# Optimization experiments

Measured on AMD Instinct MI355X. Metric: run time of the kernel, lower is better.

## Reference

```python
import jax, jax.numpy as jnp
import numpy as np


def _gcn_conv(x, src, dst, num_nodes, W, b):
    """PyG GCNConv: add self-loops, symmetric normalization, scatter-add, bias."""
    h = x @ W  # [N, F_out]
    # degree over destination nodes (all edge weights are 1, incl. self-loops)
    deg = jax.ops.segment_sum(jnp.ones_like(dst, dtype=h.dtype), dst,
                              num_segments=num_nodes)
    deg_inv_sqrt = jnp.where(deg > 0, jax.lax.rsqrt(deg), 0.0)
    norm = deg_inv_sqrt[src] * deg_inv_sqrt[dst]  # [E+N]
    msg = h[src] * norm[:, None]                  # gather + scale
    out = jax.ops.segment_sum(msg, dst, num_segments=num_nodes)  # scatter-add
    return out + b


def setup_inputs() -> dict:
    key = jax.random.key(0)
    k_x, k_e, k_w1, k_w2 = jax.random.split(key, 4)
    N, E, F = 50000, 800000, 128
    x = jax.random.normal(k_x, (N, F), dtype=jnp.float32)
    edge_index = jax.random.randint(k_e, (2, E), 0, N, dtype=jnp.int64)
    scale = 1.0 / np.sqrt(F)
    W1 = jax.random.normal(k_w1, (F, F), dtype=jnp.float32) * scale
    b1 = jnp.zeros((F,), dtype=jnp.float32)
    W2 = jax.random.normal(k_w2, (F, F), dtype=jnp.float32) * scale
    b2 = jnp.zeros((F,), dtype=jnp.float32)
    return {"x": x, "edge_index": edge_index, "W1": W1, "b1": b1,
            "W2": W2, "b2": b2}


def reference(x, edge_index, W1, b1, W2, b2):
    num_nodes = x.shape[0]
    loops = jnp.arange(num_nodes, dtype=edge_index.dtype)
    src = jnp.concatenate([edge_index[0], loops])
    dst = jnp.concatenate([edge_index[1], loops])
    # layer 1: GCNConv -> Identity norm -> relu -> dropout(eval=identity)
    h = jax.nn.relu(_gcn_conv(x, src, dst, num_nodes, W1, b1))
    # layer 2 (last_activation=True, so relu again)
    out = jax.nn.relu(_gcn_conv(h, src, dst, num_nodes, W2, b2))
    return out
```

## Files before the change

kernel.cpp:

```cpp
#include <hip/hip_runtime.h>
#include <hip/hip_bf16.h>

#define CDIV(a,b) (((a)+(b)-1)/(b))

typedef __bf16 bf16x8 __attribute__((ext_vector_type(8)));
typedef float  f32x4  __attribute__((ext_vector_type(4)));

union Frag16 { uint4 u; bf16x8 f; unsigned short s[8]; };
union Pack8  { unsigned short s[4]; uint2 u; };

__device__ __forceinline__ unsigned short f2bf(float f) {
    unsigned u = __float_as_uint(f);
    return (unsigned short)((u + 0x7fff + ((u >> 16) & 1)) >> 16);
}
__device__ __forceinline__ float bf2f(unsigned short s) {
    return __uint_as_float(((unsigned)s) << 16);
}

__device__ __forceinline__ int load_src(const int* e, int f, int E, int i) {
    return f ? e[i] : e[2 * i];
}
__device__ __forceinline__ int load_dst(const int* e, int f, int E, int i) {
    return f ? e[E + i] : e[2 * (E + i)];
}

__global__ __launch_bounds__(256) void prep_kernel(const float* __restrict__ W1,
                                                   const float* __restrict__ W2,
                                                   unsigned short* __restrict__ Wf1h,
                                                   unsigned short* __restrict__ Wf1l,
                                                   unsigned short* __restrict__ Wf2h,
                                                   unsigned short* __restrict__ Wf2l,
                                                   const int* __restrict__ edges,
                                                   int* __restrict__ flag, int E,
                                                   int4* __restrict__ zero_base, int Z4) {
    int tid = threadIdx.x;
    if (blockIdx.x == 2) {
        if (tid == 0) *flag = 0;
        __syncthreads();
        int n = min(E, 4096);
        int found = 0;
        for (int j = tid; j < n; j += 256) found |= (edges[2 * j + 1] != 0);
        if (found) *flag = 1;
        return;
    }
    if (blockIdx.x >= 3) {
        int idx = (blockIdx.x - 3) * 256 + tid;
        if (idx < Z4) zero_base[idx] = make_int4(0, 0, 0, 0);
        return;
    }
    const float* W = (blockIdx.x == 0) ? W1 : W2;
    unsigned short* Wfh = (blockIdx.x == 0) ? Wf1h : Wf2h;
    unsigned short* Wfl = (blockIdx.x == 0) ? Wf1l : Wf2l;
    #pragma unroll
    for (int it = 0; it < 8; ++it) {
        int c = it * 256 + tid;
        int ntk = c >> 6;
        int lane = c & 63;
        int ks = ntk & 3;
        int ntile = ntk >> 2;
        int quad = lane >> 4, nlo = lane & 15;
        int n = ntile * 16 + nlo;
        Frag16 h, l;
        #pragma unroll
        for (int j = 0; j < 8; ++j) {
            float w = W[(ks * 32 + quad * 8 + j) * 128 + n];
            h.s[j] = f2bf(w);
            float rr = w - bf2f(h.s[j]);
            l.s[j] = f2bf(rr);
        }
        *(uint4*)(Wfh + (size_t)c * 8) = h.u;
        *(uint4*)(Wfl + (size_t)c * 8) = l.u;
    }
}

__device__ __forceinline__ void gemm_body(const float* __restrict__ X,
                                          const unsigned short* __restrict__ Wfh,
                                          const unsigned short* __restrict__ Wfl,
                                          unsigned short* __restrict__ out16,
                                          int N, int blk,
                                          unsigned short (*Xh)[136],
                                          unsigned short (*Xl)[136]) {
    int tid = threadIdx.x;
    int row0 = blk * 64;
    #pragma unroll
    for (int it = 0; it < 8; ++it) {
        int f = it * 256 + tid;
        int r = f >> 5, c4 = f & 31;
        float4 v = make_float4(0.f, 0.f, 0.f, 0.f);
        int gr = row0 + r;
        if (gr < N) v = *(const float4*)(X + (size_t)gr * 128 + c4 * 4);
        float vv[4] = {v.x, v.y, v.z, v.w};
        Pack8 h, l;
        #pragma unroll
        for (int j = 0; j < 4; ++j) {
            h.s[j] = f2bf(vv[j]);
            float rr = vv[j] - bf2f(h.s[j]);
            l.s[j] = f2bf(rr);
        }
        *(uint2*)(&Xh[r][c4 * 4]) = h.u;
        *(uint2*)(&Xl[r][c4 * 4]) = l.u;
    }
    __syncthreads();

    int lane = tid & 63;
    int wv = tid >> 6;
    int quad = lane >> 4, nlo = lane & 15;
    f32x4 acc[8];
    #pragma unroll
    for (int t = 0; t < 8; ++t) acc[t] = (f32x4){0.f, 0.f, 0.f, 0.f};

    #pragma unroll
    for (int ks = 0; ks < 4; ++ks) {
        int kcol = ks * 32 + quad * 8;
        Frag16 xh, xl;
        xh.u = *(const uint4*)(&Xh[wv * 16 + nlo][kcol]);
        xl.u = *(const uint4*)(&Xl[wv * 16 + nlo][kcol]);
        #pragma unroll
        for (int t = 0; t < 8; ++t) {
            size_t cidx = ((size_t)(t * 4 + ks) * 64 + lane) * 8;
            Frag16 wh, wl;
            wh.u = *(const uint4*)(Wfh + cidx);
            wl.u = *(const uint4*)(Wfl + cidx);
            acc[t] = __builtin_amdgcn_mfma_f32_16x16x32_bf16(xh.f, wh.f, acc[t], 0, 0, 0);
            acc[t] = __builtin_amdgcn_mfma_f32_16x16x32_bf16(xh.f, wl.f, acc[t], 0, 0, 0);
            acc[t] = __builtin_amdgcn_mfma_f32_16x16x32_bf16(xl.f, wh.f, acc[t], 0, 0, 0);
        }
    }
    #pragma unroll
    for (int rg = 0; rg < 4; ++rg) {
        int gr = row0 + wv * 16 + quad * 4 + rg;
        if (gr < N) {
            #pragma unroll
            for (int t = 0; t < 8; ++t)
                out16[(size_t)gr * 128 + t * 16 + nlo] = f2bf(acc[t][rg]);
        }
    }
}

__global__ __launch_bounds__(256) void fat_kernel(const float* __restrict__ X,
                                                  const unsigned short* __restrict__ Wfh,
                                                  const unsigned short* __restrict__ Wfl,
                                                  unsigned short* __restrict__ out16,
                                                  int N, int Ggemm,
                                                  const int* __restrict__ edges,
                                                  const int* __restrict__ flag,
                                                  int* __restrict__ counts_sh,
                                                  int* __restrict__ rank, int E) {
    __shared__ unsigned short Xh[64][136];
    __shared__ unsigned short Xl[64][136];
    if (blockIdx.x < (unsigned)Ggemm) {
        gemm_body(X, Wfh, Wfl, out16, N, blockIdx.x, Xh, Xl);
        return;
    }
    int e = (blockIdx.x - Ggemm) * 256 + threadIdx.x;
    if (e >= E) return;
    int f = *flag;
    int d = load_dst(edges, f, E, e);
    int s = blockIdx.x & 7;
    int r = atomicAdd(&counts_sh[s * N + d], 1);
    rank[e] = (r << 3) | s;
}

__global__ __launch_bounds__(256) void gemm_h1_kernel(const unsigned short* __restrict__ H1,
                                                      const unsigned short* __restrict__ Wfh,
                                                      const unsigned short* __restrict__ Wfl,
                                                      unsigned short* __restrict__ out16,
                                                      int N) {
    int tid = threadIdx.x;
    int lane = tid & 63, wv = tid >> 6;
    int quad = lane >> 4, nlo = lane & 15;
    int row0 = blockIdx.x * 64 + wv * 16;
    int arow = min(row0 + nlo, N - 1);
    Frag16 xa[4];
    #pragma unroll
    for (int ks = 0; ks < 4; ++ks)
        xa[ks].u = *(const uint4*)(H1 + (size_t)arow * 128 + ks * 32 + quad * 8);

    f32x4 acc[8];
    #pragma unroll
    for (int t = 0; t < 8; ++t) acc[t] = (f32x4){0.f, 0.f, 0.f, 0.f};

    #pragma unroll
    for (int ks = 0; ks < 4; ++ks) {
        #pragma unroll
        for (int t = 0; t < 8; ++t) {
            size_t cidx = ((size_t)(t * 4 + ks) * 64 + lane) * 8;
            Frag16 wh, wl;
            wh.u = *(const uint4*)(Wfh + cidx);
            wl.u = *(const uint4*)(Wfl + cidx);
            acc[t] = __builtin_amdgcn_mfma_f32_16x16x32_bf16(xa[ks].f, wh.f, acc[t], 0, 0, 0);
            acc[t] = __builtin_amdgcn_mfma_f32_16x16x32_bf16(xa[ks].f, wl.f, acc[t], 0, 0, 0);
        }
    }
    #pragma unroll
    for (int rg = 0; rg < 4; ++rg) {
        int gr = row0 + quad * 4 + rg;
        if (gr < N) {
            #pragma unroll
            for (int t = 0; t < 8; ++t)
                out16[(size_t)gr * 128 + t * 16 + nlo] = f2bf(acc[t][rg]);
        }
    }
}

__global__ __launch_bounds__(256) void merge_dis_kernel(int* __restrict__ counts_sh,
                                                        int* __restrict__ counts,
                                                        float* __restrict__ dis,
                                                        int* __restrict__ bsum, int N) {
    __shared__ int red[4];
    int tid = threadIdx.x;
    int bs = 0;
    #pragma unroll
    for (int j = 0; j < 4; ++j) {
        int d = blockIdx.x * 1024 + j * 256 + tid;
        if (d < N) {
            int run = 0;
            #pragma unroll
            for (int s = 0; s < 8; ++s) {
                int v = counts_sh[s * N + d];
                counts_sh[s * N + d] = run;
                run += v;
            }
            counts[d] = run;
            dis[d] = rsqrtf((float)(run + 1));
            bs += run;
        }
    }
    #pragma unroll
    for (int off = 32; off >= 1; off >>= 1) bs += __shfl_down(bs, off, 64);
    if ((tid & 63) == 0) red[tid >> 6] = bs;
    __syncthreads();
    if (tid == 0) bsum[blockIdx.x] = red[0] + red[1] + red[2] + red[3];
}

__global__ void scan2_kernel(const int* __restrict__ bsum, int* __restrict__ boff,
                             int B, int* __restrict__ row_ptr, int N, int E) {
    int lane = threadIdx.x;
    int carry = 0;
    for (int base = 0; base < B; base += 64) {
        int i = base + lane;
        int v = (i < B) ? bsum[i] : 0;
        int x = v;
        #pragma unroll
        for (int off = 1; off < 64; off <<= 1) {
            int t = __shfl_up(x, off, 64);
            if (lane >= off) x += t;
        }
        if (i < B) boff[i] = carry + x - v;
        carry += __shfl(x, 63, 64);
    }
    if (lane == 0) row_ptr[N] = E;
}

__global__ __launch_bounds__(256) void scan3_kernel(const int* __restrict__ counts,
                                                    const int* __restrict__ boff,
                                                    int* __restrict__ row_ptr, int N) {
    __shared__ int wsum[4];
    int tid = threadIdx.x;
    int lane = tid & 63, wv = tid >> 6;
    int base = blockIdx.x * 1024 + tid * 4;
    int c[4];
    #pragma unroll
    for (int j = 0; j < 4; ++j) c[j] = (base + j < N) ? counts[base + j] : 0;
    int tsum = c[0] + c[1] + c[2] + c[3];
    int x = tsum;
    #pragma unroll
    for (int off = 1; off < 64; off <<= 1) {
        int t = __shfl_up(x, off, 64);
        if (lane >= off) x += t;
    }
    int texcl = x - tsum;
    if (lane == 63) wsum[wv] = x;
    __syncthreads();
    int woff = 0;
    for (int w = 0; w < wv; ++w) woff += wsum[w];
    int off0 = boff[blockIdx.x] + woff + texcl;
    int run = 0;
    #pragma unroll
    for (int j = 0; j < 4; ++j) {
        if (base + j < N) row_ptr[base + j] = off0 + run;
        run += c[j];
    }
}

__global__ void fill_kernel(const int* __restrict__ edges, const int* __restrict__ flag,
                            const int* __restrict__ row_ptr, const int* __restrict__ rank,
                            const int* __restrict__ counts_sh,
                            const float* __restrict__ dis, int2* __restrict__ edata,
                            int E, int N) {
    int e = blockIdx.x * blockDim.x + threadIdx.x;
    if (e >= E) return;
    int f = *flag;
    int s = load_src(edges, f, E, e);
    int d = load_dst(edges, f, E, e);
    int rk = rank[e];
    int sh = rk & 7;
    int pos = row_ptr[d] + counts_sh[sh * N + d] + (rk >> 3);
    edata[pos] = make_int2(s, __float_as_int(dis[s]));
}

template <bool BF16OUT>
__global__ __launch_bounds__(256) void agg_kernel(const unsigned short* __restrict__ H16,
                                                  const int* __restrict__ row_ptr,
                                                  const int2* __restrict__ edata,
                                                  const float* __restrict__ dis,
                                                  const float* __restrict__ bias,
                                                  void* __restrict__ outp, int N) {
    int wid = (blockIdx.x * blockDim.x + threadIdx.x) >> 6;
    int lane = threadIdx.x & 63;
    if (wid >= N) return;
    const ushort2* H2 = (const ushort2*)H16;
    float dd = dis[wid];
    ushort2 hv = H2[(size_t)wid * 64 + lane];
    float wself = dd * dd;
    float2 acc = make_float2(bf2f(hv.x) * wself, bf2f(hv.y) * wself);
    int e0 = __builtin_amdgcn_readfirstlane(row_ptr[wid]);
    int e1 = __builtin_amdgcn_readfirstlane(row_ptr[wid + 1]);
    for (int e = e0; e < e1; e += 8) {
        int rem = e1 - e;
        int   sj[8];
        float wj[8];
        #pragma unroll
        for (int j = 0; j < 8; ++j) {
            bool valid = j < rem;
            int2 ed = edata[valid ? e + j : e];
            sj[j] = ed.x;
            wj[j] = valid ? __int_as_float(ed.y) * dd : 0.f;
        }
        ushort2 aj[8];
        #pragma unroll
        for (int j = 0; j < 8; ++j)
            aj[j] = H2[(size_t)sj[j] * 64 + lane];
        #pragma unroll
        for (int j = 0; j < 8; ++j) {
            acc.x += bf2f(aj[j].x) * wj[j];
            acc.y += bf2f(aj[j].y) * wj[j];
        }
    }
    float2 b = ((const float2*)bias)[lane];
    float ox = fmaxf(acc.x + b.x, 0.f);
    float oy = fmaxf(acc.y + b.y, 0.f);
    if (BF16OUT) {
        ushort2 o = make_ushort2(f2bf(ox), f2bf(oy));
        ((ushort2*)outp)[(size_t)wid * 64 + lane] = o;
    } else {
        ((float2*)outp)[(size_t)wid * 64 + lane] = make_float2(ox, oy);
    }
}

extern "C" void kernel_launch(void* const* d_in, const int* in_sizes, int n_in,
                              void* d_out, int out_size, void* d_ws, size_t ws_size,
                              hipStream_t stream) {
    const float* x    = (const float*)d_in[0];
    const int*  edges = (const int*)d_in[1];
    const float* W1   = (const float*)d_in[2];
    const float* b1   = (const float*)d_in[3];
    const float* W2   = (const float*)d_in[4];
    const float* b2   = (const float*)d_in[5];
    float* out = (float*)d_out;

    const int F = 128;
    const int N = in_sizes[0] / F;
    const int E = in_sizes[1] / 2;
    const int NB = CDIV(N, 1024);
    const int Ggemm = CDIV(N, 64);
    const int Gcount = CDIV(E, 256);

    #define AL4(v) (((v) + 3) & ~3)
    unsigned short* A16 = (unsigned short*)d_ws;
    unsigned short* H1  = A16 + (size_t)AL4(N * F);
    float* dis      = (float*)(H1 + (size_t)AL4(N * F));
    int*  counts    = (int*)(dis + AL4(N));
    int*  counts_sh = counts + AL4(N);
    int*  flag      = counts_sh + AL4(8 * N);
    int*  row_ptr   = flag + 4;
    int*  bsum      = row_ptr + AL4(N + 1);
    int*  boff      = bsum + 64;
    int*  rank      = boff + 64;
    int2* edata     = (int2*)(rank + AL4(E));
    unsigned short* Wf1h = (unsigned short*)(edata + E);
    unsigned short* Wf1l = Wf1h + 16384;
    unsigned short* Wf2h = Wf1l + 16384;
    unsigned short* Wf2l = Wf2h + 16384;

    const int Z4 = AL4(8 * N) / 4;
    const int Gprep = 3 + CDIV(Z4, 256);

    prep_kernel<<<Gprep, 256, 0, stream>>>(W1, W2, Wf1h, Wf1l, Wf2h, Wf2l,
                                           edges, flag, E, (int4*)counts_sh, Z4);
    fat_kernel<<<Ggemm + Gcount, 256, 0, stream>>>(x, Wf1h, Wf1l, A16, N, Ggemm,
                                                   edges, flag, counts_sh, rank, E);
    merge_dis_kernel<<<NB, 256, 0, stream>>>(counts_sh, counts, dis, bsum, N);
    scan2_kernel<<<1, 64, 0, stream>>>(bsum, boff, NB, row_ptr, N, E);
    scan3_kernel<<<NB, 256, 0, stream>>>(counts, boff, row_ptr, N);
    fill_kernel<<<Gcount, 256, 0, stream>>>(edges, flag, row_ptr, rank,
                                            counts_sh, dis, edata, E, N);

    agg_kernel<true><<<CDIV(N * 64, 256), 256, 0, stream>>>(A16, row_ptr, edata, dis, b1, H1, N);
    gemm_h1_kernel<<<CDIV(N, 64), 256, 0, stream>>>(H1, Wf2h, Wf2l, A16, N);
    agg_kernel<false><<<CDIV(N * 64, 256), 256, 0, stream>>>(A16, row_ptr, edata, dis, b2, out, N);
}
```

Baseline: 222.8 us.

## Partition bf16 feature matrices into column slabs and aggregate per slab

The bf16 intermediates are now stored as four column slabs of 32 features each (slab-major), written that way by both GEMMs and read that way by the second GEMM. The aggregation kernel is split into four passes by blockIdx, one per slab. In each pass a wave processes one node, and each 16-lane group handles a different edge, so a gathered row is 64 bytes and the wave covers 8 edges per iteration. Partial sums are combined with cross-lane shuffles. The aim is to make the random neighbour gathers hit a smaller working set (one slab, about 3.2 MB), which fits better in cache, at the cost of reading the edge list four times and adding shuffle reductions.

```diff
diff --git a/kernel.cpp b/kernel.cpp
--- a/kernel.cpp
+++ b/kernel.cpp
@@ -132,7 +132,8 @@
         if (gr < N) {
             #pragma unroll
             for (int t = 0; t < 8; ++t)
-                out16[(size_t)gr * 128 + t * 16 + nlo] = f2bf(acc[t][rg]);
+                out16[((size_t)(t >> 1) * N + gr) * 32 + (t & 1) * 16 + nlo] =
+                    f2bf(acc[t][rg]);
         }
     }
 }
@@ -174,7 +175,7 @@
     Frag16 xa[4];
     #pragma unroll
     for (int ks = 0; ks < 4; ++ks)
-        xa[ks].u = *(const uint4*)(H1 + (size_t)arow * 128 + ks * 32 + quad * 8);
+        xa[ks].u = *(const uint4*)(H1 + ((size_t)ks * N + arow) * 32 + quad * 8);
 
     f32x4 acc[8];
     #pragma unroll
@@ -198,7 +199,8 @@
         if (gr < N) {
             #pragma unroll
             for (int t = 0; t < 8; ++t)
-                out16[(size_t)gr * 128 + t * 16 + nlo] = f2bf(acc[t][rg]);
+                out16[((size_t)(t >> 1) * N + gr) * 32 + (t & 1) * 16 + nlo] =
+                    f2bf(acc[t][rg]);
         }
     }
 }
@@ -305,46 +307,50 @@
                                                   const int2* __restrict__ edata,
                                                   const float* __restrict__ dis,
                                                   const float* __restrict__ bias,
-                                                  void* __restrict__ outp, int N) {
-    int wid = (blockIdx.x * blockDim.x + threadIdx.x) >> 6;
+                                                  void* __restrict__ outp, int N, int Bq) {
+    int q   = blockIdx.x / Bq;
+    int bi  = blockIdx.x - q * Bq;
+    int wv  = threadIdx.x >> 6;
     int lane = threadIdx.x & 63;
+    int wid = bi * 4 + wv;
     if (wid >= N) return;
+    int g = lane >> 4, fl = lane & 15;
+    int q16 = q * 16;
     const ushort2* H2 = (const ushort2*)H16;
     float dd = dis[wid];
-    ushort2 hv = H2[(size_t)wid * 64 + lane];
-    float wself = dd * dd;
-    float2 acc = make_float2(bf2f(hv.x) * wself, bf2f(hv.y) * wself);
+    ushort2 hv = H2[((size_t)q * N + wid) * 16 + fl];
+    float ws = (g == 0) ? dd * dd : 0.f;
+    float2 acc = make_float2(bf2f(hv.x) * ws, bf2f(hv.y) * ws);
     int e0 = __builtin_amdgcn_readfirstlane(row_ptr[wid]);
     int e1 = __builtin_amdgcn_readfirstlane(row_ptr[wid + 1]);
-    for (int e = e0; e < e1; e += 8) {
-        int rem = e1 - e;
-        int   sj[8];
-        float wj[8];
-        #pragma unroll
-        for (int j = 0; j < 8; ++j) {
-            bool valid = j < rem;
-            int2 ed = edata[valid ? e + j : e];
-            sj[j] = ed.x;
-            wj[j] = valid ? __int_as_float(ed.y) * dd : 0.f;
-        }
-        ushort2 aj[8];
-        #pragma unroll
-        for (int j = 0; j < 8; ++j)
-            aj[j] = H2[(size_t)sj[j] * 64 + lane];
-        #pragma unroll
-        for (int j = 0; j < 8; ++j) {
-            acc.x += bf2f(aj[j].x) * wj[j];
-            acc.y += bf2f(aj[j].y) * wj[j];
-        }
-    }
-    float2 b = ((const float2*)bias)[lane];
+    for (int base = e0; base < e1; base += 8) {
+        int ea = base + g;
+        int eb = base + 4 + g;
+        bool va = ea < e1, vb = eb < e1;
+        int2 eda = edata[va ? ea : base];
+        int2 edb = edata[vb ? eb : base];
+        float wa = va ? __int_as_float(eda.y) * dd : 0.f;
+        float wb = vb ? __int_as_float(edb.y) * dd : 0.f;
+        ushort2 ha = H2[((size_t)q * N + eda.x) * 16 + fl];
+        ushort2 hb = H2[((size_t)q * N + edb.x) * 16 + fl];
+        acc.x += bf2f(ha.x) * wa;
+        acc.y += bf2f(ha.y) * wa;
+        acc.x += bf2f(hb.x) * wb;
+        acc.y += bf2f(hb.y) * wb;
+    }
+    acc.x += __shfl_xor(acc.x, 16, 64);
+    acc.y += __shfl_xor(acc.y, 16, 64);
+    acc.x += __shfl_xor(acc.x, 32, 64);
+    acc.y += __shfl_xor(acc.y, 32, 64);
+    if (g != 0) return;
+    float2 b = ((const float2*)bias)[q16 + fl];
     float ox = fmaxf(acc.x + b.x, 0.f);
     float oy = fmaxf(acc.y + b.y, 0.f);
     if (BF16OUT) {
-        ushort2 o = make_ushort2(f2bf(ox), f2bf(oy));
-        ((ushort2*)outp)[(size_t)wid * 64 + lane] = o;
+        ((ushort2*)outp)[((size_t)q * N + wid) * 16 + fl] =
+            make_ushort2(f2bf(ox), f2bf(oy));
     } else {
-        ((float2*)outp)[(size_t)wid * 64 + lane] = make_float2(ox, oy);
+        ((float2*)outp)[(size_t)wid * 64 + q16 + fl] = make_float2(ox, oy);
     }
 }
 
@@ -385,6 +391,7 @@
 
     const int Z4 = AL4(8 * N) / 4;
     const int Gprep = 3 + CDIV(Z4, 256);
+    const int Bq = CDIV(N, 4);
 
     prep_kernel<<<Gprep, 256, 0, stream>>>(W1, W2, Wf1h, Wf1l, Wf2h, Wf2l,
                                            edges, flag, E, (int4*)counts_sh, Z4);
@@ -396,7 +403,7 @@
     fill_kernel<<<Gcount, 256, 0, stream>>>(edges, flag, row_ptr, rank,
                                             counts_sh, dis, edata, E, N);
 
-    agg_kernel<true><<<CDIV(N * 64, 256), 256, 0, stream>>>(A16, row_ptr, edata, dis, b1, H1, N);
+    agg_kernel<true><<<4 * Bq, 256, 0, stream>>>(A16, row_ptr, edata, dis, b1, H1, N, Bq);
     gemm_h1_kernel<<<CDIV(N, 64), 256, 0, stream>>>(H1, Wf2h, Wf2l, A16, N);
-    agg_kernel<false><<<CDIV(N * 64, 256), 256, 0, stream>>>(A16, row_ptr, edata, dis, b2, out, N);
-}
+    agg_kernel<false><<<4 * Bq, 256, 0, stream>>>(A16, row_ptr, edata, dis, b2, out, N, Bq);
+}
```

New measurement: 319.9 us. 43.6% more time.

## Fuse layer-1 aggregation with layer-2 GEMM through shared memory

Applied to the files above, without the earlier changes.

The layer-1 aggregation kernel now runs 16 waves per block, each aggregating one node. It writes the relu'd bf16 row into a swizzled LDS tile, and then 8 waves run the 16x128 MFMA GEMM against W2 directly from LDS. This removes the separate gemm_h1 launch and the global round trip of the intermediate H1. In exchange it uses 1024-thread blocks with a barrier, so waves on short edge lists sit idle until the slowest node in the block finishes, and half the waves do no GEMM work.

```diff
diff --git a/kernel.cpp b/kernel.cpp
--- a/kernel.cpp
+++ b/kernel.cpp
@@ -161,48 +161,6 @@
     rank[e] = (r << 3) | s;
 }
 
-__global__ __launch_bounds__(256) void gemm_h1_kernel(const unsigned short* __restrict__ H1,
-                                                      const unsigned short* __restrict__ Wfh,
-                                                      const unsigned short* __restrict__ Wfl,
-                                                      unsigned short* __restrict__ out16,
-                                                      int N) {
-    int tid = threadIdx.x;
-    int lane = tid & 63, wv = tid >> 6;
-    int quad = lane >> 4, nlo = lane & 15;
-    int row0 = blockIdx.x * 64 + wv * 16;
-    int arow = min(row0 + nlo, N - 1);
-    Frag16 xa[4];
-    #pragma unroll
-    for (int ks = 0; ks < 4; ++ks)
-        xa[ks].u = *(const uint4*)(H1 + (size_t)arow * 128 + ks * 32 + quad * 8);
-
-    f32x4 acc[8];
-    #pragma unroll
-    for (int t = 0; t < 8; ++t) acc[t] = (f32x4){0.f, 0.f, 0.f, 0.f};
-
-    #pragma unroll
-    for (int ks = 0; ks < 4; ++ks) {
-        #pragma unroll
-        for (int t = 0; t < 8; ++t) {
-            size_t cidx = ((size_t)(t * 4 + ks) * 64 + lane) * 8;
-            Frag16 wh, wl;
-            wh.u = *(const uint4*)(Wfh + cidx);
-            wl.u = *(const uint4*)(Wfl + cidx);
-            acc[t] = __builtin_amdgcn_mfma_f32_16x16x32_bf16(xa[ks].f, wh.f, acc[t], 0, 0, 0);
-            acc[t] = __builtin_amdgcn_mfma_f32_16x16x32_bf16(xa[ks].f, wl.f, acc[t], 0, 0, 0);
-        }
-    }
-    #pragma unroll
-    for (int rg = 0; rg < 4; ++rg) {
-        int gr = row0 + quad * 4 + rg;
-        if (gr < N) {
-            #pragma unroll
-            for (int t = 0; t < 8; ++t)
-                out16[(size_t)gr * 128 + t * 16 + nlo] = f2bf(acc[t][rg]);
-        }
-    }
-}
-
 __global__ __launch_bounds__(256) void merge_dis_kernel(int* __restrict__ counts_sh,
                                                         int* __restrict__ counts,
                                                         float* __restrict__ dis,
@@ -299,13 +257,83 @@
     edata[pos] = make_int2(s, __float_as_int(dis[s]));
 }
 
-template <bool BF16OUT>
-__global__ __launch_bounds__(256) void agg_kernel(const unsigned short* __restrict__ H16,
-                                                  const int* __restrict__ row_ptr,
-                                                  const int2* __restrict__ edata,
-                                                  const float* __restrict__ dis,
-                                                  const float* __restrict__ bias,
-                                                  void* __restrict__ outp, int N) {
+__global__ __launch_bounds__(1024) void agg1_fused_kernel(
+        const unsigned short* __restrict__ A16,
+        const int* __restrict__ row_ptr,
+        const int2* __restrict__ edata,
+        const float* __restrict__ dis,
+        const float* __restrict__ bias,
+        const unsigned short* __restrict__ Wfh,
+        const unsigned short* __restrict__ Wfl,
+        unsigned short* __restrict__ H1out, int N) {
+    __shared__ unsigned short Hl[16][128];
+    int wv = threadIdx.x >> 6;
+    int lane = threadIdx.x & 63;
+    int wid = blockIdx.x * 16 + wv;
+    if (wid < N) {
+        const ushort2* H2 = (const ushort2*)A16;
+        float dd = dis[wid];
+        ushort2 hv = H2[(size_t)wid * 64 + lane];
+        float wself = dd * dd;
+        float2 acc = make_float2(bf2f(hv.x) * wself, bf2f(hv.y) * wself);
+        int e0 = __builtin_amdgcn_readfirstlane(row_ptr[wid]);
+        int e1 = __builtin_amdgcn_readfirstlane(row_ptr[wid + 1]);
+        for (int e = e0; e < e1; e += 8) {
+            int rem = e1 - e;
+            int   sj[8];
+            float wj[8];
+            #pragma unroll
+            for (int j = 0; j < 8; ++j) {
+                bool valid = j < rem;
+                int2 ed = edata[valid ? e + j : e];
+                sj[j] = ed.x;
+                wj[j] = valid ? __int_as_float(ed.y) * dd : 0.f;
+            }
+            ushort2 aj[8];
+            #pragma unroll
+            for (int j = 0; j < 8; ++j)
+                aj[j] = H2[(size_t)sj[j] * 64 + lane];
+            #pragma unroll
+            for (int j = 0; j < 8; ++j) {
+                acc.x += bf2f(aj[j].x) * wj[j];
+                acc.y += bf2f(aj[j].y) * wj[j];
+            }
+        }
+        float2 b = ((const float2*)bias)[lane];
+        float ox = fmaxf(acc.x + b.x, 0.f);
+        float oy = fmaxf(acc.y + b.y, 0.f);
+        int c = (lane * 2) ^ ((wv & 7) << 3);
+        *(ushort2*)(&Hl[wv][c]) = make_ushort2(f2bf(ox), f2bf(oy));
+    }
+    __syncthreads();
+    if (wv >= 8) return;
+    int quad = lane >> 4, nlo = lane & 15;
+    f32x4 acc = (f32x4){0.f, 0.f, 0.f, 0.f};
+    #pragma unroll
+    for (int ks = 0; ks < 4; ++ks) {
+        int cb = (ks * 32 + quad * 8) ^ ((nlo & 7) << 3);
+        Frag16 xa, wh, wl;
+        xa.u = *(const uint4*)(&Hl[nlo][cb]);
+        size_t cidx = ((size_t)(wv * 4 + ks) * 64 + lane) * 8;
+        wh.u = *(const uint4*)(Wfh + cidx);
+        wl.u = *(const uint4*)(Wfl + cidx);
+        acc = __builtin_amdgcn_mfma_f32_16x16x32_bf16(xa.f, wh.f, acc, 0, 0, 0);
+        acc = __builtin_amdgcn_mfma_f32_16x16x32_bf16(xa.f, wl.f, acc, 0, 0, 0);
+    }
+    #pragma unroll
+    for (int rg = 0; rg < 4; ++rg) {
+        int gr = blockIdx.x * 16 + quad * 4 + rg;
+        if (gr < N)
+            H1out[(size_t)gr * 128 + wv * 16 + nlo] = f2bf(acc[rg]);
+    }
+}
+
+__global__ __launch_bounds__(256) void agg2_kernel(const unsigned short* __restrict__ H16,
+                                                   const int* __restrict__ row_ptr,
+                                                   const int2* __restrict__ edata,
+                                                   const float* __restrict__ dis,
+                                                   const float* __restrict__ bias,
+                                                   float* __restrict__ outp, int N) {
     int wid = (blockIdx.x * blockDim.x + threadIdx.x) >> 6;
     int lane = threadIdx.x & 63;
     if (wid >= N) return;
@@ -340,12 +368,7 @@
     float2 b = ((const float2*)bias)[lane];
     float ox = fmaxf(acc.x + b.x, 0.f);
     float oy = fmaxf(acc.y + b.y, 0.f);
-    if (BF16OUT) {
-        ushort2 o = make_ushort2(f2bf(ox), f2bf(oy));
-        ((ushort2*)outp)[(size_t)wid * 64 + lane] = o;
-    } else {
-        ((float2*)outp)[(size_t)wid * 64 + lane] = make_float2(ox, oy);
-    }
+    ((float2*)outp)[(size_t)wid * 64 + lane] = make_float2(ox, oy);
 }
 
 extern "C" void kernel_launch(void* const* d_in, const int* in_sizes, int n_in,
@@ -396,7 +419,7 @@
     fill_kernel<<<Gcount, 256, 0, stream>>>(edges, flag, row_ptr, rank,
                                             counts_sh, dis, edata, E, N);
 
-    agg_kernel<true><<<CDIV(N * 64, 256), 256, 0, stream>>>(A16, row_ptr, edata, dis, b1, H1, N);
-    gemm_h1_kernel<<<CDIV(N, 64), 256, 0, stream>>>(H1, Wf2h, Wf2l, A16, N);
-    agg_kernel<false><<<CDIV(N * 64, 256), 256, 0, stream>>>(A16, row_ptr, edata, dis, b2, out, N);
-}
+    agg1_fused_kernel<<<CDIV(N, 16), 1024, 0, stream>>>(A16, row_ptr, edata, dis,
+                                                        b1, Wf2h, Wf2l, H1, N);
+    agg2_kernel<<<CDIV(N * 64, 256), 256, 0, stream>>>(H1, row_ptr, edata, dis, b2, out, N);
+}
```

New measurement: 217.2 us. 2.5% less time.
